# Optimization experiments

Measured on AMD Instinct MI355X. Metric: run time of the kernel, lower is better.

The kernel has to match this reference:

```python
import jax, jax.numpy as jnp
import numpy as np

VW, VD, VH = 96, 96, 96  # voxel_width, voxel_depth, voxel_height


def _grid_points():
    # voxel centers mapped to [-1, 1]: (2*i + 1 - N) / N
    xp = (2.0 * jnp.arange(VW) + 1.0 - VW) / VW
    yp = (2.0 * jnp.arange(VD) + 1.0 - VD) / VD
    zp = (2.0 * jnp.arange(VH) + 1.0 - VH) / VH
    X, Y, Z = jnp.meshgrid(xp, yp, zp, indexing='ij')
    return jnp.stack([X.ravel(), Y.ravel(), Z.ravel()], axis=-1)  # (V, 3)


def setup_inputs() -> dict:
    key = jax.random.key(0)
    k1, k2 = jax.random.split(key)
    B, NV, NF = 8, 2048, 512
    vertices = jax.random.uniform(k1, (B, NV, 3), dtype=jnp.float32, minval=-1.0, maxval=1.0)
    facets = jax.random.randint(k2, (B, NF, 4), 0, NV, dtype=jnp.int64)
    return {"vertices": vertices, "facets": facets}


def reference(vertices, facets):
    # vertices: (B, NV, 3) float32; facets: (B, NF, 4) int indices into vertices
    B = vertices.shape[0]
    NF = facets.shape[1]
    # vertices_to_facets: per-batch gather -> (B, NF, 4, 3)
    fverts = jax.vmap(lambda v, f: v[f])(vertices, facets)
    P = _grid_points()                      # (V, 3) voxel centers
    V = P.shape[0]

    def step(idx_map, xs):
        fi, verts = xs                      # verts: (B, 4, 3)
        v3 = verts[:, 3]                    # (B, 3)
        # T[:, j] = verts[j] - verts[3]  (columns are tetra edges)
        T = jnp.swapaxes(verts[:, :3] - v3[:, None, :], 1, 2)  # (B, 3, 3)
        a, b, c = T[:, 0, 0], T[:, 0, 1], T[:, 0, 2]
        d, e, f = T[:, 1, 0], T[:, 1, 1], T[:, 1, 2]
        g, h, i = T[:, 2, 0], T[:, 2, 1], T[:, 2, 2]
        # adjugate of T (matches t_inv_* in the original)
        adj = jnp.stack([
            jnp.stack([e * i - f * h, c * h - b * i, b * f - c * e], axis=-1),
            jnp.stack([f * g - d * i, a * i - c * g, c * d - a * f], axis=-1),
            jnp.stack([d * h - e * g, b * g - a * h, a * e - b * d], axis=-1),
        ], axis=1)                          # (B, 3, 3)
        det = a * (e * i - f * h) - b * (d * i - f * g) + c * (d * h - e * g)  # (B,)
        dvec = P[None, :, :] - v3[:, None, :]                  # (B, V, 3)
        lam = jnp.einsum('brc,bvc->bvr', adj, dvec) / det[:, None, None]  # (B, V, 3)
        lam4 = 1.0 - lam.sum(axis=-1, keepdims=True)
        lams = jnp.concatenate([lam, lam4], axis=-1)           # (B, V, 4)
        # original skips when any lambda < 0 or > 1 (strict) -> inside is inclusive
        inside = jnp.all((lams >= 0.0) & (lams <= 1.0), axis=-1)  # (B, V)
        idx_map = jnp.where((idx_map < 0) & inside, fi, idx_map)
        return idx_map, None

    idx0 = jnp.full((B, V), -1, dtype=jnp.int32)
    xs = (jnp.arange(NF, dtype=jnp.int32), jnp.swapaxes(fverts, 0, 1))
    idx_map, _ = jax.lax.scan(step, idx0, xs)
    alpha = (idx_map >= 0).astype(jnp.float32).reshape(B, VW, VD, VH)
    return alpha
```

## Files before the change

kernel.cpp:

```cpp
#include <hip/hip_runtime.h>

#pragma clang fp contract(off)

#define VWD 96
#define NVERT 2048
#define NFAC 512
#define NBATCH 8
#define NSLAB 3456
#define RECF 16
#define CULC 94

#define CUL(c, b, f) cul[(size_t)(c) * (NBATCH * NFAC) + (size_t)(b) * NFAC + (f)]

__global__ __launch_bounds__(512) void precompute_kernel(
    const float* __restrict__ vertices,
    const int*   __restrict__ facets,
    float*       __restrict__ cul,
    float*       __restrict__ body)
{
    __shared__ unsigned skey[NFAC];
    const int b = blockIdx.x;
    const int j = threadIdx.x;
    const float* vb = vertices + (size_t)b * NVERT * 3;

    int4 fi = ((const int4*)facets)[b * NFAC + j];
    float x0 = vb[3*fi.x+0], y0 = vb[3*fi.x+1], z0 = vb[3*fi.x+2];
    float x1 = vb[3*fi.y+0], y1 = vb[3*fi.y+1], z1 = vb[3*fi.y+2];
    float x2 = vb[3*fi.z+0], y2 = vb[3*fi.z+1], z2 = vb[3*fi.z+2];
    float x3 = vb[3*fi.w+0], y3 = vb[3*fi.w+1], z3 = vb[3*fi.w+2];
    float a  = x0-x3, bb = x1-x3, c  = x2-x3;
    float d  = y0-y3, e  = y1-y3, f  = y2-y3;
    float g  = z0-z3, h  = z1-z3, ii = z2-z3;
    float A00 = e*ii - f*h,  A01 = c*h  - bb*ii, A02 = bb*f - c*e;
    float A10 = f*g  - d*ii, A11 = a*ii - c*g,   A12 = c*d  - a*f;
    float A20 = d*h  - e*g,  A21 = bb*g - a*h,   A22 = a*e  - bb*d;
    float det = a*(e*ii - f*h) - bb*(d*ii - f*g) + c*(d*h - e*g);
    if (det < 0.0f) {
        det = -det;
        A00 = -A00; A01 = -A01; A02 = -A02;
        A10 = -A10; A11 = -A11; A12 = -A12;
        A20 = -A20; A21 = -A21; A22 = -A22;
    }
    unsigned myk = ~__float_as_uint(det);
    skey[j] = myk;
    __syncthreads();

    int rank = 0;
    const uint4* sk4 = (const uint4*)skey;
    for (int k0 = 0; k0 < NFAC; k0 += 4) {
        uint4 kk = sk4[k0 >> 2];
        rank += (kk.x < myk) + ((kk.x == myk) & (k0 + 0 < j));
        rank += (kk.y < myk) + ((kk.y == myk) & (k0 + 1 < j));
        rank += (kk.z < myk) + ((kk.z == myk) & (k0 + 2 < j));
        rank += (kk.w < myk) + ((kk.w == myk) & (k0 + 3 < j));
    }

    CUL(0, b, rank) = fminf(fminf(x0,x1),fminf(x2,x3)) - 1e-4f;
    CUL(1, b, rank) = fminf(fminf(y0,y1),fminf(y2,y3)) - 1e-4f;
    CUL(2, b, rank) = fminf(fminf(z0,z1),fminf(z2,z3)) - 1e-4f;
    CUL(3, b, rank) = fmaxf(fmaxf(x0,x1),fmaxf(x2,x3)) + 1e-4f;
    CUL(4, b, rank) = fmaxf(fmaxf(y0,y1),fmaxf(y2,y3)) + 1e-4f;
    CUL(5, b, rank) = fmaxf(fmaxf(z0,z1),fmaxf(z2,z3)) + 1e-4f;

    const float HX = 7.0f/96.0f, HZ = 3.0f/96.0f;
    auto plane = [&](float pax, float pay, float paz,
                     float pbx, float pby, float pbz,
                     float pcx, float pcy, float pcz,
                     float pox, float poy, float poz, int base) {
        float e1x = pbx-pax, e1y = pby-pay, e1z = pbz-paz;
        float e2x = pcx-pax, e2y = pcy-pay, e2z = pcz-paz;
        float nx = e1y*e2z - e1z*e2y;
        float ny = e1z*e2x - e1x*e2z;
        float nz = e1x*e2y - e1y*e2x;
        float sdot = nx*(pox-pax) + ny*(poy-pay) + nz*(poz-paz);
        if (sdot > 0.0f) { nx=-nx; ny=-ny; nz=-nz; sdot=-sdot; }
        float dpl = nx*pax + ny*pay + nz*paz;
        float n1s = fabsf(nx)+fabsf(ny)+fabsf(nz);
        float M = 1e-4f*(-sdot) + 1e-4f*n1s + 1e-4f;
        float rhs = dpl + M + (fabsf(nx)*HX + fabsf(ny)*HX + fabsf(nz)*HZ);
        CUL(base+0, b, rank) = nx;
        CUL(base+1, b, rank) = ny;
        CUL(base+2, b, rank) = nz;
        CUL(base+3, b, rank) = rhs;
    };
    plane(x1,y1,z1, x2,y2,z2, x3,y3,z3, x0,y0,z0, 6);
    plane(x0,y0,z0, x2,y2,z2, x3,y3,z3, x1,y1,z1, 10);
    plane(x0,y0,z0, x1,y1,z1, x3,y3,z3, x2,y2,z2, 14);
    plane(x0,y0,z0, x1,y1,z1, x2,y2,z2, x3,y3,z3, 18);

    auto axis = [&](float c1, float c2,
                    float t0, float t1, float t2, float t3,
                    float r, int base) {
        float tmin = fminf(fminf(t0,t1), fminf(t2,t3));
        float tmax = fmaxf(fmaxf(t0,t1), fmaxf(t2,t3));
        float M = 1e-4f*(fabsf(c1)+fabsf(c2)) + 1e-5f;
        CUL(base+0, b, rank) = c1;
        CUL(base+1, b, rank) = c2;
        CUL(base+2, b, rank) = tmin - r - M;
        CUL(base+3, b, rank) = tmax + r + M;
    };
    auto edge = [&](float xA, float yA, float zA,
                    float xB, float yB, float zB, int base) {
        float ex = xB-xA, ey = yB-yA, ez = zB-zA;
        axis(ez, -ey,
             ez*y0 - ey*z0, ez*y1 - ey*z1, ez*y2 - ey*z2, ez*y3 - ey*z3,
             fabsf(ez)*HX + fabsf(ey)*HZ, base+0);
        axis(-ez, ex,
             ex*z0 - ez*x0, ex*z1 - ez*x1, ex*z2 - ez*x2, ex*z3 - ez*x3,
             fabsf(ez)*HX + fabsf(ex)*HZ, base+4);
        axis(ey, -ex,
             ey*x0 - ex*y0, ey*x1 - ex*y1, ey*x2 - ex*y2, ey*x3 - ex*y3,
             fabsf(ey)*HX + fabsf(ex)*HX, base+8);
    };
    edge(x0,y0,z0, x1,y1,z1, 22 + 0*12);
    edge(x0,y0,z0, x2,y2,z2, 22 + 1*12);
    edge(x0,y0,z0, x3,y3,z3, 22 + 2*12);
    edge(x1,y1,z1, x2,y2,z2, 22 + 3*12);
    edge(x1,y1,z1, x3,y3,z3, 22 + 4*12);
    edge(x2,y2,z2, x3,y3,z3, 22 + 5*12);

    float* bo = body + ((size_t)b * NFAC + rank) * RECF;
    bo[0]  = det; bo[1]  = x3;  bo[2]  = y3;  bo[3]  = z3;
    bo[4]  = A00; bo[5]  = A01; bo[6]  = A02; bo[7]  = A10;
    bo[8]  = A11; bo[9]  = A12; bo[10] = A20; bo[11] = A21;
    bo[12] = A22;
    bo[13] = det * (1.0f - 1e-5f) - 1e-25f;
    bo[14] = det * (1.0f + 1e-5f) + 1e-25f;
    bo[15] = 0.0f;
}

__global__ __launch_bounds__(512) void mask_kernel(
    const float* __restrict__ cul,
    unsigned long long* __restrict__ masks)
{
    const int col = blockIdx.x;
    const int b   = blockIdx.y;
    const int f   = threadIdx.x;
    const int w   = threadIdx.x >> 6;

    const int sx = col / 12, sy = col % 12;
    const float cx = (float)(16*sx + 8 - VWD) / 96.0f;
    const float cy = (float)(16*sy + 8 - VWD) / 96.0f;

    float bminx=CUL(0,b,f), bminy=CUL(1,b,f), bminz=CUL(2,b,f);
    float bmaxx=CUL(3,b,f), bmaxy=CUL(4,b,f), bmaxz=CUL(5,b,f);

    const float colminx = (float)(16*sx + 1  - VWD) / 96.0f;
    const float colmaxx = (float)(16*sx + 15 - VWD) / 96.0f;
    const float colminy = (float)(16*sy + 1  - VWD) / 96.0f;
    const float colmaxy = (float)(16*sy + 15 - VWD) / 96.0f;
    bool ovxy = (bminx <= colmaxx) & (bmaxx >= colminx) &
                (bminy <= colmaxy) & (bmaxy >= colminy);

#pragma unroll
    for (int e = 0; e < 6; ++e) {
        float c1 = CUL(22 + e*12 + 8,  b, f);
        float c2 = CUL(22 + e*12 + 9,  b, f);
        float lo = CUL(22 + e*12 + 10, b, f);
        float hi = CUL(22 + e*12 + 11, b, f);
        float dd = c1*cx + c2*cy;
        ovxy = ovxy & (dd >= lo) & (dd <= hi);
    }

    const float cz0   = (float)(4 - VWD) / 96.0f;
    const float stepc = 8.0f / 96.0f;
    float tlo = -1.0f, thi = 24.0f;

    auto addc = [&](float dd, float es, float lo, float hi) {
        bool  tiny  = fabsf(es) < 1e-7f;
        float esafe = tiny ? 1.0f : es;
        float r  = 1.0f / esafe;
        float av = (lo - dd) * r;
        float bv = (hi - dd) * r;
        float t0 = fminf(av, bv) - 1e-3f;
        float t1 = fmaxf(av, bv) + 1e-3f;
        bool ok_tiny = (dd >= lo - 3e-6f) & (dd <= hi + 3e-6f);
        t0 = tiny ? (ok_tiny ? -1.0f : 1e9f)  : t0;
        t1 = tiny ? (ok_tiny ? 25.0f : -1e9f) : t1;
        tlo = fmaxf(tlo, t0);
        thi = fminf(thi, t1);
    };

#pragma unroll
    for (int p = 0; p < 4; ++p) {
        float nx = CUL(6+p*4+0, b, f);
        float ny = CUL(6+p*4+1, b, f);
        float nz = CUL(6+p*4+2, b, f);
        float rh = CUL(6+p*4+3, b, f);
        float dd = nx*cx + ny*cy + nz*cz0 - rh;
        addc(dd, nz*stepc, -1e30f, 0.0f);
    }

#pragma unroll
    for (int e = 0; e < 6; ++e) {
#pragma unroll
        for (int t = 0; t < 2; ++t) {
            int base = 22 + e*12 + t*4;
            float c1 = CUL(base+0, b, f);
            float c2 = CUL(base+1, b, f);
            float lo = CUL(base+2, b, f);
            float hi = CUL(base+3, b, f);
            float dd = c1 * (t == 0 ? cy : cx) + c2 * cz0;
            addc(dd, c2*stepc, lo, hi);
        }
    }

    const float zlo0 = (float)(1 - VWD) / 96.0f;
    const float zhi0 = (float)(7 - VWD) / 96.0f;
    tlo = fmaxf(tlo, (bminz - zhi0) * 12.0f - 1e-3f);
    thi = fminf(thi, (bmaxz - zlo0) * 12.0f + 1e-3f);

    int ilo = (int)ceilf(fmaxf(fminf(tlo, 1e8f), -1.0f));
    int ihi = (int)floorf(fminf(fmaxf(thi, -1e8f), 24.0f));

    unsigned long long* mp = masks + ((size_t)b * NSLAB + (size_t)col * 24) * 8 + w;
#pragma unroll 4
    for (int sz = 0; sz < 24; ++sz) {
        bool ov = ovxy & (sz >= ilo) & (sz <= ihi);
        unsigned long long bal = __ballot((int)ov);
        if ((threadIdx.x & 63) == 0) mp[(size_t)sz * 8] = bal;
    }
}

__global__ __launch_bounds__(128) void voxelize_kernel(
    const float*              __restrict__ body,
    const unsigned long long* __restrict__ masks,
    float*                    __restrict__ out)
{
    const int b    = blockIdx.y;
    const int wave = threadIdx.x >> 6;
    const int lane = threadIdx.x & 63;
    const int slab = blockIdx.x * 2 + wave;
    const int sz = slab % 24;
    const int sy = (slab / 24) % 12;
    const int sx = slab / 288;
    const int ix  = sx*8 + (lane >> 3);
    const int iy  = sy*8 + (lane & 7);
    const int iz0 = sz*4;

    const float px  = (float)(2*ix + 1 - VWD) / 96.0f;
    const float py  = (float)(2*iy + 1 - VWD) / 96.0f;
    const float pz0 = (float)(2*(iz0+0) + 1 - VWD) / 96.0f;
    const float pz1 = (float)(2*(iz0+1) + 1 - VWD) / 96.0f;
    const float pz2 = (float)(2*(iz0+2) + 1 - VWD) / 96.0f;
    const float pz3 = (float)(2*(iz0+3) + 1 - VWD) / 96.0f;

    const unsigned long long* mp = masks + ((size_t)b * NSLAB + slab) * 8;
    const float* bb = body + (size_t)b * NFAC * RECF;

    unsigned fnd = 0u;
    for (int w = 0; w < 8; ++w) {
        unsigned long long m = mp[w];
        while (m) {
            int bit = __builtin_ctzll(m);
            m &= m - 1;
            int f = __builtin_amdgcn_readfirstlane(w * 64 + bit);
            const float* bo = bb + f * RECF;
            float det = bo[0], v3x = bo[1], v3y = bo[2], v3z = bo[3];
            float A00 = bo[4],  A01 = bo[5],  A02 = bo[6],  A10 = bo[7];
            float A11 = bo[8],  A12 = bo[9],  A20 = bo[10], A21 = bo[11];
            float A22 = bo[12], dhi = bo[13], mhi = bo[14];
            float dx = px - v3x, dy = py - v3y;
            float p0 = A00*dx + A01*dy;
            float p1 = A10*dx + A11*dy;
            float p2 = A20*dx + A21*dy;
            float dzk0 = pz0 - v3z, dzk1 = pz1 - v3z;
            float dzk2 = pz2 - v3z, dzk3 = pz3 - v3z;
            unsigned need = 0u;
#pragma unroll
            for (int k = 0; k < 4; ++k) {
                float dzk = (k == 0) ? dzk0 : (k == 1) ? dzk1
                          : (k == 2) ? dzk2 : dzk3;
                float n0 = p0 + A02*dzk;
                float n1 = p1 + A12*dzk;
                float n2 = p2 + A22*dzk;
                float sm = (n0 + n1) + n2;
                float mn = fminf(fminf(n0, n1), n2);
                bool ge0 = (mn >= 0.0f);
                bool def = ge0 & (sm <= dhi);
                bool may = ge0 & (sm <= mhi);
                if (may & !def & !((fnd >> k) & 1u)) need |= (1u << k);
                if (def) fnd |= (1u << k);
            }
            if (__any(need != 0u)) {
#pragma unroll
                for (int k = 0; k < 4; ++k) {
                    float dzk = (k == 0) ? dzk0 : (k == 1) ? dzk1
                              : (k == 2) ? dzk2 : dzk3;
                    float n0 = p0 + A02*dzk;
                    float n1 = p1 + A12*dzk;
                    float n2 = p2 + A22*dzk;
                    float l0 = n0 / det;
                    float l1 = n1 / det;
                    float l2 = n2 / det;
                    float l3 = 1.0f - ((l0 + l1) + l2);
                    bool inside = (l0 >= 0.0f) & (l0 <= 1.0f) &
                                  (l1 >= 0.0f) & (l1 <= 1.0f) &
                                  (l2 >= 0.0f) & (l2 <= 1.0f) &
                                  (l3 >= 0.0f) & (l3 <= 1.0f);
                    if (((need >> k) & 1u) & inside) fnd |= (1u << k);
                }
            }
            if (__all(fnd == 15u)) goto done;
        }
    }
done:
    float4 v;
    v.x = (fnd & 1u) ? 1.0f : 0.0f;
    v.y = (fnd & 2u) ? 1.0f : 0.0f;
    v.z = (fnd & 4u) ? 1.0f : 0.0f;
    v.w = (fnd & 8u) ? 1.0f : 0.0f;
    *(float4*)&out[(size_t)b*(VWD*VWD*VWD) + (size_t)ix*(VWD*VWD) + iy*VWD + iz0] = v;
}

extern "C" void kernel_launch(void* const* d_in, const int* in_sizes, int n_in,
                              void* d_out, int out_size, void* d_ws, size_t ws_size,
                              hipStream_t stream) {
    const float* vertices = (const float*)d_in[0];
    const int*   facets   = (const int*)d_in[1];
    float*       out      = (float*)d_out;

    float* cul  = (float*)d_ws;
    float* body = (float*)((char*)d_ws + (size_t)CULC * NBATCH * NFAC * 4);
    unsigned long long* msk =
        (unsigned long long*)((char*)d_ws +
                              (size_t)(CULC + RECF) * NBATCH * NFAC * 4);

    precompute_kernel<<<NBATCH, 512, 0, stream>>>(vertices, facets, cul, body);
    mask_kernel<<<dim3(144, NBATCH), 512, 0, stream>>>(cul, msk);
    dim3 grid(NSLAB / 2, NBATCH);
    voxelize_kernel<<<grid, 128, 0, stream>>>(body, msk, out);
}
```

Measured before the change: 150.8 us.

## Precompute per-facet z-interval coefficients to drop divisions from mask kernel

Moves the per-constraint division by the z-step coefficient out of the mask kernel and into the per-facet precompute. Each constraint is stored pre-normalised as slope and offset terms plus widened bounds, and the culling record shrinks from 94 to 82 floats. The mask kernel then needs only a multiply-subtract and a min/max per constraint. The cost is a different rounding path, covered by added slack margins, and the tiny-coefficient case is now clamped instead of handled explicitly, which could change conservativeness.

Result: no change. 150.6 us (-0.2%).

```diff
diff --git a/kernel.cpp b/kernel.cpp
--- a/kernel.cpp
+++ b/kernel.cpp
@@ -8,7 +8,7 @@
 #define NBATCH 8
 #define NSLAB 3456
 #define RECF 16
-#define CULC 94
+#define CULC 82
 
 #define CUL(c, b, f) cul[(size_t)(c) * (NBATCH * NFAC) + (size_t)(b) * NFAC + (f)]
 
@@ -63,6 +63,14 @@
     CUL(5, b, rank) = fmaxf(fmaxf(z0,z1),fmaxf(z2,z3)) + 1e-4f;
 
     const float HX = 7.0f/96.0f, HZ = 3.0f/96.0f;
+    const float cz0   = (float)(4 - VWD) / 96.0f;
+    const float stepc = 8.0f / 96.0f;
+
+    auto safediv = [](float num, float es) {
+        float esafe = (es >= 0.0f) ? fmaxf(es, 1e-7f) : fminf(es, -1e-7f);
+        return num / esafe;
+    };
+
     auto plane = [&](float pax, float pay, float paz,
                      float pbx, float pby, float pbz,
                      float pcx, float pcy, float pcz,
@@ -78,19 +86,25 @@
         float n1s = fabsf(nx)+fabsf(ny)+fabsf(nz);
         float M = 1e-4f*(-sdot) + 1e-4f*n1s + 1e-4f;
         float rhs = dpl + M + (fabsf(nx)*HX + fabsf(ny)*HX + fabsf(nz)*HZ);
-        CUL(base+0, b, rank) = nx;
-        CUL(base+1, b, rank) = ny;
-        CUL(base+2, b, rank) = nz;
-        CUL(base+3, b, rank) = rhs;
-    };
-    plane(x1,y1,z1, x2,y2,z2, x3,y3,z3, x0,y0,z0, 6);
-    plane(x0,y0,z0, x2,y2,z2, x3,y3,z3, x1,y1,z1, 10);
-    plane(x0,y0,z0, x1,y1,z1, x3,y3,z3, x2,y2,z2, 14);
-    plane(x0,y0,z0, x1,y1,z1, x2,y2,z2, x3,y3,z3, 18);
-
-    auto axis = [&](float c1, float c2,
-                    float t0, float t1, float t2, float t3,
-                    float r, int base) {
+        float es = nz * stepc;
+        float P  = safediv(nx, es);
+        float Q  = safediv(ny, es);
+        float C  = safediv(rhs - nz*cz0, es);
+        float SL = 1e-2f + 1e-6f*(fabsf(C)+fabsf(P)+fabsf(Q));
+        bool pos = (es >= 0.0f);
+        CUL(base+0, b, rank) = P;
+        CUL(base+1, b, rank) = Q;
+        CUL(base+2, b, rank) = pos ? -1e30f : (C - SL);
+        CUL(base+3, b, rank) = pos ? (C + SL) : 1e30f;
+    };
+    plane(x1,y1,z1, x2,y2,z2, x3,y3,z3, x0,y0,z0, 30);
+    plane(x0,y0,z0, x2,y2,z2, x3,y3,z3, x1,y1,z1, 34);
+    plane(x0,y0,z0, x1,y1,z1, x3,y3,z3, x2,y2,z2, 38);
+    plane(x0,y0,z0, x1,y1,z1, x2,y2,z2, x3,y3,z3, 42);
+
+    auto zaxis = [&](float c1, float c2,
+                     float t0, float t1, float t2, float t3,
+                     float r, int base) {
         float tmin = fminf(fminf(t0,t1), fminf(t2,t3));
         float tmax = fmaxf(fmaxf(t0,t1), fmaxf(t2,t3));
         float M = 1e-4f*(fabsf(c1)+fabsf(c2)) + 1e-5f;
@@ -99,25 +113,42 @@
         CUL(base+2, b, rank) = tmin - r - M;
         CUL(base+3, b, rank) = tmax + r + M;
     };
+    auto vaxis = [&](float c1, float c2,
+                     float t0, float t1, float t2, float t3,
+                     float r, int base) {
+        float tmin = fminf(fminf(t0,t1), fminf(t2,t3));
+        float tmax = fmaxf(fmaxf(t0,t1), fmaxf(t2,t3));
+        float M  = 1e-4f*(fabsf(c1)+fabsf(c2)) + 1e-5f;
+        float lo = tmin - r - M;
+        float hi = tmax + r + M;
+        float es = c2 * stepc;
+        float K  = safediv(c1, es);
+        float L1 = safediv(lo - c2*cz0, es);
+        float L2 = safediv(hi - c2*cz0, es);
+        float SL = 1e-2f + 1e-6f*(fabsf(L1)+fabsf(L2)+fabsf(K));
+        CUL(base+0, b, rank) = K;
+        CUL(base+1, b, rank) = fminf(L1, L2) - SL;
+        CUL(base+2, b, rank) = fmaxf(L1, L2) + SL;
+    };
     auto edge = [&](float xA, float yA, float zA,
-                    float xB, float yB, float zB, int base) {
+                    float xB, float yB, float zB, int ei) {
         float ex = xB-xA, ey = yB-yA, ez = zB-zA;
-        axis(ez, -ey,
-             ez*y0 - ey*z0, ez*y1 - ey*z1, ez*y2 - ey*z2, ez*y3 - ey*z3,
-             fabsf(ez)*HX + fabsf(ey)*HZ, base+0);
-        axis(-ez, ex,
-             ex*z0 - ez*x0, ex*z1 - ez*x1, ex*z2 - ez*x2, ex*z3 - ez*x3,
-             fabsf(ez)*HX + fabsf(ex)*HZ, base+4);
-        axis(ey, -ex,
-             ey*x0 - ex*y0, ey*x1 - ex*y1, ey*x2 - ex*y2, ey*x3 - ex*y3,
-             fabsf(ey)*HX + fabsf(ex)*HX, base+8);
-    };
-    edge(x0,y0,z0, x1,y1,z1, 22 + 0*12);
-    edge(x0,y0,z0, x2,y2,z2, 22 + 1*12);
-    edge(x0,y0,z0, x3,y3,z3, 22 + 2*12);
-    edge(x1,y1,z1, x2,y2,z2, 22 + 3*12);
-    edge(x1,y1,z1, x3,y3,z3, 22 + 4*12);
-    edge(x2,y2,z2, x3,y3,z3, 22 + 5*12);
+        vaxis(ez, -ey,
+              ez*y0 - ey*z0, ez*y1 - ey*z1, ez*y2 - ey*z2, ez*y3 - ey*z3,
+              fabsf(ez)*HX + fabsf(ey)*HZ, 46 + ei*3);
+        vaxis(-ez, ex,
+              ex*z0 - ez*x0, ex*z1 - ez*x1, ex*z2 - ez*x2, ex*z3 - ez*x3,
+              fabsf(ez)*HX + fabsf(ex)*HZ, 64 + ei*3);
+        zaxis(ey, -ex,
+              ey*x0 - ex*y0, ey*x1 - ex*y1, ey*x2 - ex*y2, ey*x3 - ex*y3,
+              fabsf(ey)*HX + fabsf(ex)*HX, 6 + ei*4);
+    };
+    edge(x0,y0,z0, x1,y1,z1, 0);
+    edge(x0,y0,z0, x2,y2,z2, 1);
+    edge(x0,y0,z0, x3,y3,z3, 2);
+    edge(x1,y1,z1, x2,y2,z2, 3);
+    edge(x1,y1,z1, x3,y3,z3, 4);
+    edge(x2,y2,z2, x3,y3,z3, 5);
 
     float* bo = body + ((size_t)b * NFAC + rank) * RECF;
     bo[0]  = det; bo[1]  = x3;  bo[2]  = y3;  bo[3]  = z3;
@@ -154,55 +185,44 @@
 
 #pragma unroll
     for (int e = 0; e < 6; ++e) {
-        float c1 = CUL(22 + e*12 + 8,  b, f);
-        float c2 = CUL(22 + e*12 + 9,  b, f);
-        float lo = CUL(22 + e*12 + 10, b, f);
-        float hi = CUL(22 + e*12 + 11, b, f);
+        float c1 = CUL(6 + e*4 + 0, b, f);
+        float c2 = CUL(6 + e*4 + 1, b, f);
+        float lo = CUL(6 + e*4 + 2, b, f);
+        float hi = CUL(6 + e*4 + 3, b, f);
         float dd = c1*cx + c2*cy;
         ovxy = ovxy & (dd >= lo) & (dd <= hi);
     }
 
-    const float cz0   = (float)(4 - VWD) / 96.0f;
-    const float stepc = 8.0f / 96.0f;
     float tlo = -1.0f, thi = 24.0f;
 
-    auto addc = [&](float dd, float es, float lo, float hi) {
-        bool  tiny  = fabsf(es) < 1e-7f;
-        float esafe = tiny ? 1.0f : es;
-        float r  = 1.0f / esafe;
-        float av = (lo - dd) * r;
-        float bv = (hi - dd) * r;
-        float t0 = fminf(av, bv) - 1e-3f;
-        float t1 = fmaxf(av, bv) + 1e-3f;
-        bool ok_tiny = (dd >= lo - 3e-6f) & (dd <= hi + 3e-6f);
-        t0 = tiny ? (ok_tiny ? -1.0f : 1e9f)  : t0;
-        t1 = tiny ? (ok_tiny ? 25.0f : -1e9f) : t1;
-        tlo = fmaxf(tlo, t0);
-        thi = fminf(thi, t1);
-    };
-
 #pragma unroll
     for (int p = 0; p < 4; ++p) {
-        float nx = CUL(6+p*4+0, b, f);
-        float ny = CUL(6+p*4+1, b, f);
-        float nz = CUL(6+p*4+2, b, f);
-        float rh = CUL(6+p*4+3, b, f);
-        float dd = nx*cx + ny*cy + nz*cz0 - rh;
-        addc(dd, nz*stepc, -1e30f, 0.0f);
+        float P   = CUL(30+p*4+0, b, f);
+        float Q   = CUL(30+p*4+1, b, f);
+        float CLO = CUL(30+p*4+2, b, f);
+        float CHI = CUL(30+p*4+3, b, f);
+        float T2  = P*cx + Q*cy;
+        tlo = fmaxf(tlo, CLO - T2);
+        thi = fminf(thi, CHI - T2);
     }
 
 #pragma unroll
     for (int e = 0; e < 6; ++e) {
-#pragma unroll
-        for (int t = 0; t < 2; ++t) {
-            int base = 22 + e*12 + t*4;
-            float c1 = CUL(base+0, b, f);
-            float c2 = CUL(base+1, b, f);
-            float lo = CUL(base+2, b, f);
-            float hi = CUL(base+3, b, f);
-            float dd = c1 * (t == 0 ? cy : cx) + c2 * cz0;
-            addc(dd, c2*stepc, lo, hi);
-        }
+        float K  = CUL(46+e*3+0, b, f);
+        float L0 = CUL(46+e*3+1, b, f);
+        float L1 = CUL(46+e*3+2, b, f);
+        float wv = K * cy;
+        tlo = fmaxf(tlo, L0 - wv);
+        thi = fminf(thi, L1 - wv);
+    }
+#pragma unroll
+    for (int e = 0; e < 6; ++e) {
+        float K  = CUL(64+e*3+0, b, f);
+        float L0 = CUL(64+e*3+1, b, f);
+        float L1 = CUL(64+e*3+2, b, f);
+        float wv = K * cx;
+        tlo = fmaxf(tlo, L0 - wv);
+        thi = fminf(thi, L1 - wv);
     }
 
     const float zlo0 = (float)(1 - VWD) / 96.0f;
```
